# Optimization experiments

Hardware: AMD Instinct MI355X
Metric: run time of the kernel (lower is better)

Reference implementation:

```python
import jax, jax.numpy as jnp
import numpy as np

N_NODES = 100000
N_REL = 4
N_EDGES = 160000  # per relation
IN_F, HID_F, OUT_F = 128, 128, 64


def hetero_layer(x, edges, W, b):
    """Sum over relations of GraphConv (norm='both'): D_in^-1/2 A_r D_out^-1/2 X W_r + b_r."""
    N = x.shape[0]
    out = jnp.zeros((N, W.shape[2]), dtype=x.dtype)
    for r in range(W.shape[0]):  # small fixed relation count
        src = edges[r, 0]
        dst = edges[r, 1]
        ones = jnp.ones(src.shape[0], dtype=x.dtype)
        deg_out = jnp.clip(jax.ops.segment_sum(ones, src, num_segments=N), 1.0)
        deg_in = jnp.clip(jax.ops.segment_sum(ones, dst, num_segments=N), 1.0)
        # scale src features, project (W first since in_feats >= out_feats), gather, scatter-sum
        h = (x * jax.lax.rsqrt(deg_out)[:, None]) @ W[r]
        agg = jax.ops.segment_sum(h[src], dst, num_segments=N)
        out = out + agg * jax.lax.rsqrt(deg_in)[:, None] + b[r]
    return out


def setup_inputs() -> dict:
    key = jax.random.key(0)
    ks = jax.random.split(key, 6)
    x = jax.random.normal(ks[0], (N_NODES, IN_F), dtype=jnp.float32)
    edges = jax.random.randint(ks[1], (N_REL, 2, N_EDGES), 0, N_NODES, dtype=jnp.int32)
    W1 = jax.random.normal(ks[2], (N_REL, IN_F, HID_F), dtype=jnp.float32) * 0.05
    b1 = jnp.zeros((N_REL, HID_F), dtype=jnp.float32)
    W2 = jax.random.normal(ks[3], (N_REL, HID_F, OUT_F), dtype=jnp.float32) * 0.05
    b2 = jnp.zeros((N_REL, OUT_F), dtype=jnp.float32)
    return {"x": x, "edges": edges, "W1": W1, "b1": b1, "W2": W2, "b2": b2}


def reference(x, edges, W1, b1, W2, b2):
    h = jax.nn.relu(hetero_layer(x, edges, W1, b1))
    return hetero_layer(h, edges, W2, b2)
```

## Files before the change

kernel.cpp:

```cpp
#include <hip/hip_runtime.h>
#include <cstddef>
#include <cstdint>

#define NN   100000
#define NR   4
#define NE   160000
#define SCAN_B 1024
#define GEMMB 512

typedef short bf16x8 __attribute__((ext_vector_type(8)));
typedef float f32x4  __attribute__((ext_vector_type(4)));

__device__ __forceinline__ unsigned short f2bf(float f) {
  union { float f; unsigned u; } v; v.f = f;
  unsigned r = v.u + 0x7fffu + ((v.u >> 16) & 1u);
  return (unsigned short)(r >> 16);
}
__device__ __forceinline__ float bf2f(unsigned short h) {
  union { unsigned u; float f; } v; v.u = ((unsigned)h) << 16;
  return v.f;
}

__device__ __forceinline__ void gll16(const unsigned short* g, unsigned short* l) {
  __builtin_amdgcn_global_load_lds(
      (const __attribute__((address_space(1))) void*)g,
      (__attribute__((address_space(3))) void*)l, 16, 0, 0);
}

#define A_ZERO 782
#define A_NBLK (A_ZERO + 6250 + 256 + 128 + 1)
__global__ __launch_bounds__(256) void phaseA_k(const float* __restrict__ x,
                                                const float* __restrict__ W1,
                                                const float* __restrict__ W2,
                                                const float* __restrict__ b1,
                                                const float* __restrict__ b2,
                                                int* __restrict__ cnt,
                                                unsigned short* __restrict__ xb,
                                                unsigned short* __restrict__ Wt1,
                                                unsigned short* __restrict__ Wt2,
                                                float* __restrict__ bs1,
                                                float* __restrict__ bs2) {
  const int bid = blockIdx.x;
  const int t = threadIdx.x;
  if (bid < A_ZERO) {
    const int i = bid * 256 + t;
    if (i < 2 * NR * NN / 4) ((int4*)cnt)[i] = make_int4(0, 0, 0, 0);
  } else if (bid < A_ZERO + 6250) {
    const int i = (bid - A_ZERO) * 256 + t;
    const float4 a = *(const float4*)&x[(size_t)i * 8];
    const float4 b = *(const float4*)&x[(size_t)i * 8 + 4];
    unsigned short o[8];
    o[0] = f2bf(a.x); o[1] = f2bf(a.y); o[2] = f2bf(a.z); o[3] = f2bf(a.w);
    o[4] = f2bf(b.x); o[5] = f2bf(b.y); o[6] = f2bf(b.z); o[7] = f2bf(b.w);
    *(bf16x8*)&xb[(size_t)i * 8] = *(bf16x8*)o;
  } else if (bid < A_ZERO + 6250 + 256) {
    const int i = (bid - A_ZERO - 6250) * 256 + t;
    const int r = i / (128 * 128);
    const int k = (i / 128) % 128;
    const int n = i % 128;
    Wt1[((size_t)r * 128 + n) * 128 + k] = f2bf(W1[i]);
  } else if (bid < A_ZERO + 6250 + 256 + 128) {
    const int i = (bid - A_ZERO - 6250 - 256) * 256 + t;
    const int r = i / (128 * 64);
    const int k = (i / 64) % 128;
    const int n = i % 64;
    Wt2[((size_t)r * 64 + n) * 128 + k] = f2bf(W2[i]);
  } else {
    if (t < 128) bs1[t] = b1[t] + b1[128 + t] + b1[256 + t] + b1[384 + t];
    if (t < 64)  bs2[t] = b2[t] + b2[64 + t] + b2[128 + t] + b2[192 + t];
  }
}

template <int NOUT>
__device__ __forceinline__ void gemm_core(const unsigned short* __restrict__ Xb,
                                          const unsigned short* __restrict__ Wtr,
                                          unsigned short* __restrict__ Hr,
                                          int vb, unsigned short (*Xl)[64 * 128]) {
  const int t = threadIdx.x;
  const int wid = t >> 6;
  const int lane = t & 63;
  const int lg = lane >> 4;
  const int lr = lane & 15;

  constexpr int NF = (NOUT == 128) ? 4 : 2;
  const int rbase = (wid & 1) * 32;
  const int cbase = (wid >> 1) * (NOUT / 2);

  bf16x8 bw[NF][4];
#pragma unroll
  for (int nf = 0; nf < NF; ++nf)
#pragma unroll
    for (int ks = 0; ks < 4; ++ks)
      bw[nf][ks] = *(const bf16x8*)&Wtr[(size_t)(cbase + nf * 16 + lr) * 128 + ks * 32 + lg * 8];

  auto stage = [&](int buf, int tile) {
    const int row0 = tile * 64;
#pragma unroll
    for (int i = 0; i < 4; ++i) {
      const int rl = wid * 16 + i * 4 + (lane >> 4);
      int gr = row0 + rl;
      if (gr >= NN) gr = NN - 1;
      const int q = (lane & 15) ^ (rl & 7);
      gll16(&Xb[(size_t)gr * 128 + q * 8], &Xl[buf][rl * 128 + (lane & 15) * 8]);
    }
  };

  const int ntiles = (NN + 63) / 64;
  int tile = vb;
  stage(0, tile);
  __syncthreads();
  int buf = 0;

  for (; tile < ntiles; tile += 128) {
    const int nxt = tile + 128;
    if (nxt < ntiles) stage(buf ^ 1, nxt);

    f32x4 acc[2][NF];
#pragma unroll
    for (int mf = 0; mf < 2; ++mf)
#pragma unroll
      for (int nf = 0; nf < NF; ++nf) acc[mf][nf] = (f32x4){0.f, 0.f, 0.f, 0.f};

#pragma unroll
    for (int ks = 0; ks < 4; ++ks) {
#pragma unroll
      for (int mf = 0; mf < 2; ++mf) {
        const int r = rbase + mf * 16 + lr;
        const bf16x8 a =
            *(const bf16x8*)&Xl[buf][r * 128 + (((ks * 4 + lg) ^ (lr & 7)) << 3)];
#pragma unroll
        for (int nf = 0; nf < NF; ++nf)
          acc[mf][nf] = __builtin_amdgcn_mfma_f32_16x16x32_bf16(a, bw[nf][ks], acc[mf][nf], 0, 0, 0);
      }
    }

    const int row0 = tile * 64;
#pragma unroll
    for (int mf = 0; mf < 2; ++mf) {
#pragma unroll
      for (int i = 0; i < 4; ++i) {
        const int row = row0 + rbase + mf * 16 + lg * 4 + i;
        if (row < NN) {
#pragma unroll
          for (int nf = 0; nf < NF; ++nf)
            Hr[(size_t)row * NOUT + cbase + nf * 16 + lr] = f2bf(acc[mf][nf][i]);
        }
      }
    }
    __syncthreads();
    buf ^= 1;
  }
}

__device__ __forceinline__ void gemm_dual_core64(const unsigned short* __restrict__ Xb,
                                                 const unsigned short* __restrict__ W0,
                                                 const unsigned short* __restrict__ W1,
                                                 unsigned short* __restrict__ H0,
                                                 unsigned short* __restrict__ H1,
                                                 int vb, unsigned short (*Xl)[64 * 128]) {
  const int t = threadIdx.x;
  const int wid = t >> 6;
  const int lane = t & 63;
  const int lg = lane >> 4;
  const int lr = lane & 15;

  const int rbase = (wid & 1) * 32;
  const int cbase = (wid >> 1) * 32;

  bf16x8 bw[2][2][4];
#pragma unroll
  for (int nf = 0; nf < 2; ++nf)
#pragma unroll
    for (int ks = 0; ks < 4; ++ks) {
      bw[0][nf][ks] = *(const bf16x8*)&W0[(size_t)(cbase + nf * 16 + lr) * 128 + ks * 32 + lg * 8];
      bw[1][nf][ks] = *(const bf16x8*)&W1[(size_t)(cbase + nf * 16 + lr) * 128 + ks * 32 + lg * 8];
    }

  auto stage = [&](int buf, int tile) {
    const int row0 = tile * 64;
#pragma unroll
    for (int i = 0; i < 4; ++i) {
      const int rl = wid * 16 + i * 4 + (lane >> 4);
      int gr = row0 + rl;
      if (gr >= NN) gr = NN - 1;
      const int q = (lane & 15) ^ (rl & 7);
      gll16(&Xb[(size_t)gr * 128 + q * 8], &Xl[buf][rl * 128 + (lane & 15) * 8]);
    }
  };

  const int ntiles = (NN + 63) / 64;
  int tile = vb;
  stage(0, tile);
  __syncthreads();
  int buf = 0;

  for (; tile < ntiles; tile += 128) {
    const int nxt = tile + 128;
    if (nxt < ntiles) stage(buf ^ 1, nxt);

    f32x4 acc[2][2][2];
#pragma unroll
    for (int mf = 0; mf < 2; ++mf)
#pragma unroll
      for (int rel = 0; rel < 2; ++rel)
#pragma unroll
        for (int nf = 0; nf < 2; ++nf) acc[mf][rel][nf] = (f32x4){0.f, 0.f, 0.f, 0.f};

#pragma unroll
    for (int ks = 0; ks < 4; ++ks) {
#pragma unroll
      for (int mf = 0; mf < 2; ++mf) {
        const int r = rbase + mf * 16 + lr;
        const bf16x8 a =
            *(const bf16x8*)&Xl[buf][r * 128 + (((ks * 4 + lg) ^ (lr & 7)) << 3)];
#pragma unroll
        for (int rel = 0; rel < 2; ++rel)
#pragma unroll
          for (int nf = 0; nf < 2; ++nf)
            acc[mf][rel][nf] = __builtin_amdgcn_mfma_f32_16x16x32_bf16(a, bw[rel][nf][ks], acc[mf][rel][nf], 0, 0, 0);
      }
    }

    const int row0 = tile * 64;
#pragma unroll
    for (int mf = 0; mf < 2; ++mf) {
#pragma unroll
      for (int i = 0; i < 4; ++i) {
        const int row = row0 + rbase + mf * 16 + lg * 4 + i;
        if (row < NN) {
#pragma unroll
          for (int nf = 0; nf < 2; ++nf) {
            H0[(size_t)row * 64 + cbase + nf * 16 + lr] = f2bf(acc[mf][0][nf][i]);
            H1[(size_t)row * 64 + cbase + nf * 16 + lr] = f2bf(acc[mf][1][nf][i]);
          }
        }
      }
    }
    __syncthreads();
    buf ^= 1;
  }
}

__global__ __launch_bounds__(256, 2) void phaseB_k(const int* __restrict__ edges,
                                                   const unsigned short* __restrict__ xb,
                                                   const unsigned short* __restrict__ Wt1,
                                                   unsigned short* __restrict__ H,
                                                   int* __restrict__ cnt_out,
                                                   int* __restrict__ cnt_in) {
  __shared__ unsigned short Xl[2][64 * 128];
  const int bid = blockIdx.x;
  if (bid < GEMMB) {
    const int z = bid >> 7;
    gemm_core<128>(xb, Wt1 + (size_t)z * 128 * 128, H + (size_t)z * NN * 128, bid & 127, Xl);
    return;
  }
  const int idx = bid - GEMMB;
  const int r = idx / 625;
  const int e = (idx - r * 625) * 256 + threadIdx.x;
  const int s = edges[(size_t)r * 2 * NE + e];
  const int d = edges[(size_t)r * 2 * NE + NE + e];
  atomicAdd(&cnt_out[(size_t)r * NN + s], 1);
  atomicAdd(&cnt_in[(size_t)r * NN + d], 1);
}

__global__ __launch_bounds__(256, 2) void gemm_dual_k(const unsigned short* __restrict__ Xb,
                                                      const unsigned short* __restrict__ Wt,
                                                      unsigned short* __restrict__ H) {
  __shared__ unsigned short Xl[2][64 * 128];
  const int zp = blockIdx.z;
  gemm_dual_core64(Xb,
                   Wt + (size_t)(2 * zp) * 64 * 128,
                   Wt + (size_t)(2 * zp + 1) * 64 * 128,
                   H + (size_t)(2 * zp) * NN * 64,
                   H + (size_t)(2 * zp + 1) * NN * 64,
                   blockIdx.x, Xl);
}

__global__ __launch_bounds__(256) void scan1_k(const int* __restrict__ cnt_in,
                                               int* __restrict__ excl,
                                               int* __restrict__ bsum) {
  const int b = blockIdx.x, t = threadIdx.x;
  const int base = b * SCAN_B;
  int v[4]; int tl = 0;
#pragma unroll
  for (int i = 0; i < 4; ++i) {
    const int idx = base + t * 4 + i;
    int c = 0;
    if (idx < NN) {
      c = cnt_in[idx] + cnt_in[NN + idx] + cnt_in[2 * NN + idx] + cnt_in[3 * NN + idx];
    }
    v[i] = c;
    tl += c;
  }
  __shared__ int sm[256];
  sm[t] = tl;
  __syncthreads();
  for (int off = 1; off < 256; off <<= 1) {
    const int x = (t >= off) ? sm[t - off] : 0;
    __syncthreads();
    sm[t] += x;
    __syncthreads();
  }
  const int incl = sm[t];
  int run = incl - tl;
#pragma unroll
  for (int i = 0; i < 4; ++i) {
    const int idx = base + t * 4 + i;
    if (idx < NN) excl[idx] = run;
    run += v[i];
  }
  if (t == 255) bsum[b] = incl;
}

__global__ __launch_bounds__(128) void scan2_k(int* __restrict__ bsum, int nb) {
  const int t = threadIdx.x;
  __shared__ int sm[128];
  const int v = (t < nb) ? bsum[t] : 0;
  sm[t] = v;
  __syncthreads();
  for (int off = 1; off < 128; off <<= 1) {
    const int x = (t >= off) ? sm[t - off] : 0;
    __syncthreads();
    sm[t] += x;
    __syncthreads();
  }
  if (t < nb) bsum[t] = sm[t] - v;
}

__global__ __launch_bounds__(256) void scan3rs_k(const int* __restrict__ cnt,
                                                 float* __restrict__ rs,
                                                 const int* __restrict__ bsum,
                                                 int* __restrict__ row_ptr,
                                                 int* __restrict__ cursor) {
  const int bid = blockIdx.x, t = threadIdx.x;
  if (bid < 3125) {
    const int i = bid * 256 + t;
    rs[i] = rsqrtf(fmaxf((float)cnt[i], 1.0f));
  } else {
    const int i = (bid - 3125) * 256 + t;
    if (i < NN) {
      const int v = cursor[i] + bsum[i / SCAN_B];
      row_ptr[i] = v;
      cursor[i] = v;
    }
    if (i == 0) row_ptr[NN] = NR * NE;
  }
}

__global__ __launch_bounds__(256) void fill_k(const int* __restrict__ edges,
                                              const float* __restrict__ rs_out,
                                              const float* __restrict__ rs_in,
                                              int* __restrict__ cursor,
                                              int2* __restrict__ csr) {
  const int r = blockIdx.y;
  const int e = blockIdx.x * 256 + threadIdx.x;
  if (e >= NE) return;
  const int s = edges[(size_t)r * 2 * NE + e];
  const int d = edges[(size_t)r * 2 * NE + NE + e];
  const int pos = atomicAdd(&cursor[d], 1);
  const float w = rs_in[(size_t)r * NN + d] * rs_out[(size_t)r * NN + s];
  csr[pos] = make_int2(r * NN + s, __float_as_int(w));
}

__global__ __launch_bounds__(256) void gather1_k(const unsigned short* __restrict__ H,
                                                 const int* __restrict__ row_ptr,
                                                 const int2* __restrict__ csr,
                                                 const float* __restrict__ bs1,
                                                 unsigned short* __restrict__ h1b) {
  const int node = blockIdx.x * 4 + (threadIdx.x >> 6);
  const int lane = threadIdx.x & 63;
  if (node >= NN) return;
  const int g  = lane >> 4;
  const int fl = lane & 15;

  float acc[8];
#pragma unroll
  for (int j = 0; j < 8; ++j) acc[j] = 0.f;

  const int beg = row_ptr[node];
  const int end = row_ptr[node + 1];
  for (int e = beg + g; e < end; e += 4) {
    const int2 p = csr[e];
    const float w = __int_as_float(p.y);
    const bf16x8 h = *(const bf16x8*)&H[(size_t)p.x * 128 + fl * 8];
#pragma unroll
    for (int j = 0; j < 8; ++j)
      acc[j] = fmaf(bf2f((unsigned short)h[j]), w, acc[j]);
  }
#pragma unroll
  for (int j = 0; j < 8; ++j) {
    acc[j] += __shfl_xor(acc[j], 16);
    acc[j] += __shfl_xor(acc[j], 32);
  }
  if (g == 0) {
    const float4 c0 = *(const float4*)&bs1[fl * 8];
    const float4 c1 = *(const float4*)&bs1[fl * 8 + 4];
    unsigned short o[8];
    o[0] = f2bf(fmaxf(acc[0] + c0.x, 0.f));
    o[1] = f2bf(fmaxf(acc[1] + c0.y, 0.f));
    o[2] = f2bf(fmaxf(acc[2] + c0.z, 0.f));
    o[3] = f2bf(fmaxf(acc[3] + c0.w, 0.f));
    o[4] = f2bf(fmaxf(acc[4] + c1.x, 0.f));
    o[5] = f2bf(fmaxf(acc[5] + c1.y, 0.f));
    o[6] = f2bf(fmaxf(acc[6] + c1.z, 0.f));
    o[7] = f2bf(fmaxf(acc[7] + c1.w, 0.f));
    *(bf16x8*)&h1b[(size_t)node * 128 + fl * 8] = *(bf16x8*)o;
  }
}

__global__ __launch_bounds__(256) void gather2_k(const unsigned short* __restrict__ H,
                                                 const int* __restrict__ row_ptr,
                                                 const int2* __restrict__ csr,
                                                 const float* __restrict__ bs2,
                                                 float* __restrict__ out) {
  const int node = blockIdx.x * 4 + (threadIdx.x >> 6);
  const int lane = threadIdx.x & 63;
  if (node >= NN) return;
  const int g  = lane >> 3;
  const int fl = lane & 7;

  float acc[8];
#pragma unroll
  for (int j = 0; j < 8; ++j) acc[j] = 0.f;

  const int beg = row_ptr[node];
  const int end = row_ptr[node + 1];
  for (int e = beg + g; e < end; e += 8) {
    const int2 p = csr[e];
    const float w = __int_as_float(p.y);
    const bf16x8 h = *(const bf16x8*)&H[(size_t)p.x * 64 + fl * 8];
#pragma unroll
    for (int j = 0; j < 8; ++j)
      acc[j] = fmaf(bf2f((unsigned short)h[j]), w, acc[j]);
  }
#pragma unroll
  for (int j = 0; j < 8; ++j) {
    acc[j] += __shfl_xor(acc[j], 8);
    acc[j] += __shfl_xor(acc[j], 16);
    acc[j] += __shfl_xor(acc[j], 32);
  }
  if (g == 0) {
    const float4 c0 = *(const float4*)&bs2[fl * 8];
    const float4 c1 = *(const float4*)&bs2[fl * 8 + 4];
    float4 o0, o1;
    o0.x = acc[0] + c0.x; o0.y = acc[1] + c0.y; o0.z = acc[2] + c0.z; o0.w = acc[3] + c0.w;
    o1.x = acc[4] + c1.x; o1.y = acc[5] + c1.y; o1.z = acc[6] + c1.z; o1.w = acc[7] + c1.w;
    *(float4*)&out[(size_t)node * 64 + fl * 8]     = o0;
    *(float4*)&out[(size_t)node * 64 + fl * 8 + 4] = o1;
  }
}

extern "C" void kernel_launch(void* const* d_in, const int* in_sizes, int n_in,
                              void* d_out, int out_size, void* d_ws, size_t ws_size,
                              hipStream_t stream) {
  const float* x     = (const float*)d_in[0];
  const int*   edges = (const int*)d_in[1];
  const float* W1    = (const float*)d_in[2];
  const float* b1    = (const float*)d_in[3];
  const float* W2    = (const float*)d_in[4];
  const float* b2    = (const float*)d_in[5];
  float* out = (float*)d_out;

  unsigned short* xb   = (unsigned short*)d_ws;
  unsigned short* h1b  = xb;
  unsigned short* Hbuf = xb + (size_t)NN * 128;
  unsigned short* Wt1  = Hbuf + (size_t)NR * NN * 128;
  unsigned short* Wt2  = Wt1 + (size_t)NR * 128 * 128;
  float* rs_out = (float*)(Wt2 + (size_t)NR * 64 * 128);
  float* rs_in  = rs_out + (size_t)NR * NN;
  int* cnt_out  = (int*)(rs_in + (size_t)NR * NN);
  int* cnt_in   = cnt_out + (size_t)NR * NN;
  int* row_ptr  = cnt_in + (size_t)NR * NN;
  int* cursor   = row_ptr + (NN + 1);
  int* bsum     = cursor + NN;
  float* bs1    = (float*)(bsum + 128);
  float* bs2    = bs1 + 128;
  int2* csr     = (int2*)(bs2 + 64);

  const int nb = (NN + SCAN_B - 1) / SCAN_B;

  phaseA_k<<<A_NBLK, 256, 0, stream>>>(x, W1, W2, b1, b2, cnt_out, xb, Wt1, Wt2, bs1, bs2);
  phaseB_k<<<GEMMB + 2500, 256, 0, stream>>>(edges, xb, Wt1, Hbuf, cnt_out, cnt_in);
  scan1_k<<<nb, 256, 0, stream>>>(cnt_in, cursor , bsum);
  scan2_k<<<1, 128, 0, stream>>>(bsum, nb);
  scan3rs_k<<<3125 + (NN + 255) / 256, 256, 0, stream>>>(cnt_out, rs_out, bsum, row_ptr, cursor);
  fill_k<<<dim3((NE + 255) / 256, NR), 256, 0, stream>>>(edges, rs_out, rs_in, cursor, csr);
  gather1_k<<<(NN + 3) / 4, 256, 0, stream>>>(Hbuf, row_ptr, csr, bs1, h1b);
  gemm_dual_k<<<dim3(128, 1, 2), 256, 0, stream>>>(h1b, Wt2, Hbuf);
  gather2_k<<<(NN + 3) / 4, 256, 0, stream>>>(Hbuf, row_ptr, csr, bs2, out);
}
```

Baseline: 217.1 us.

## Shard degree counters across copies and use per-relation CSR fill cursors

Degree counting now spreads its atomics over four replicated counter arrays, chosen by block index, to cut same-address contention. The scan and rs kernels reduce across the shards, and the fill step uses a separate cursor per relation and destination so fewer atomics collide on one node. The CSR buffer now reuses the counter workspace, and zeroing covers four times as much memory. This adds reduction reads and a larger memset in exchange for less atomic serialization.

After: 221.1 us. About the same (+1.9%).

```diff
diff --git a/kernel.cpp b/kernel.cpp
--- a/kernel.cpp
+++ b/kernel.cpp
@@ -7,6 +7,7 @@
 #define NE   160000
 #define SCAN_B 1024
 #define GEMMB 512
+#define SH   4
 
 typedef short bf16x8 __attribute__((ext_vector_type(8)));
 typedef float f32x4  __attribute__((ext_vector_type(4)));
@@ -27,7 +28,7 @@
       (__attribute__((address_space(3))) void*)l, 16, 0, 0);
 }
 
-#define A_ZERO 782
+#define A_ZERO 3125
 #define A_NBLK (A_ZERO + 6250 + 256 + 128 + 1)
 __global__ __launch_bounds__(256) void phaseA_k(const float* __restrict__ x,
                                                 const float* __restrict__ W1,
@@ -44,7 +45,7 @@
   const int t = threadIdx.x;
   if (bid < A_ZERO) {
     const int i = bid * 256 + t;
-    if (i < 2 * NR * NN / 4) ((int4*)cnt)[i] = make_int4(0, 0, 0, 0);
+    ((int4*)cnt)[i] = make_int4(0, 0, 0, 0);
   } else if (bid < A_ZERO + 6250) {
     const int i = (bid - A_ZERO) * 256 + t;
     const float4 a = *(const float4*)&x[(size_t)i * 8];
@@ -245,8 +246,8 @@
                                                    const unsigned short* __restrict__ xb,
                                                    const unsigned short* __restrict__ Wt1,
                                                    unsigned short* __restrict__ H,
-                                                   int* __restrict__ cnt_out,
-                                                   int* __restrict__ cnt_in) {
+                                                   int* __restrict__ cntO,
+                                                   int* __restrict__ cntI) {
   __shared__ unsigned short Xl[2][64 * 128];
   const int bid = blockIdx.x;
   if (bid < GEMMB) {
@@ -256,11 +257,12 @@
   }
   const int idx = bid - GEMMB;
   const int r = idx / 625;
+  const int sh = idx & (SH - 1);
   const int e = (idx - r * 625) * 256 + threadIdx.x;
   const int s = edges[(size_t)r * 2 * NE + e];
   const int d = edges[(size_t)r * 2 * NE + NE + e];
-  atomicAdd(&cnt_out[(size_t)r * NN + s], 1);
-  atomicAdd(&cnt_in[(size_t)r * NN + d], 1);
+  atomicAdd(&cntO[((size_t)sh * NR + r) * NN + s], 1);
+  atomicAdd(&cntI[((size_t)sh * NR + r) * NN + d], 1);
 }
 
 __global__ __launch_bounds__(256, 2) void gemm_dual_k(const unsigned short* __restrict__ Xb,
@@ -276,7 +278,7 @@
                    blockIdx.x, Xl);
 }
 
-__global__ __launch_bounds__(256) void scan1_k(const int* __restrict__ cnt_in,
+__global__ __launch_bounds__(256) void scan1_k(const int* __restrict__ cntI,
                                                int* __restrict__ excl,
                                                int* __restrict__ bsum) {
   const int b = blockIdx.x, t = threadIdx.x;
@@ -287,7 +289,11 @@
     const int idx = base + t * 4 + i;
     int c = 0;
     if (idx < NN) {
-      c = cnt_in[idx] + cnt_in[NN + idx] + cnt_in[2 * NN + idx] + cnt_in[3 * NN + idx];
+#pragma unroll
+      for (int sh = 0; sh < SH; ++sh) {
+        const size_t o = (size_t)sh * NR * NN + idx;
+        c += cntI[o] + cntI[o + NN] + cntI[o + 2 * NN] + cntI[o + 3 * NN];
+      }
     }
     v[i] = c;
     tl += c;
@@ -327,21 +333,46 @@
   if (t < nb) bsum[t] = sm[t] - v;
 }
 
-__global__ __launch_bounds__(256) void scan3rs_k(const int* __restrict__ cnt,
-                                                 float* __restrict__ rs,
+__global__ __launch_bounds__(256) void scan3rs_k(const int* __restrict__ cntO,
+                                                 const int* __restrict__ cntI,
+                                                 float* __restrict__ rs_out,
+                                                 float* __restrict__ rs_in,
+                                                 const int* __restrict__ excl,
                                                  const int* __restrict__ bsum,
                                                  int* __restrict__ row_ptr,
-                                                 int* __restrict__ cursor) {
+                                                 int* __restrict__ cursorR) {
   const int bid = blockIdx.x, t = threadIdx.x;
   if (bid < 3125) {
     const int i = bid * 256 + t;
-    rs[i] = rsqrtf(fmaxf((float)cnt[i], 1.0f));
+    if (i < NR * NN) {
+      int c = 0;
+#pragma unroll
+      for (int sh = 0; sh < SH; ++sh) c += cntO[(size_t)sh * NR * NN + i];
+      rs_out[i] = rsqrtf(fmaxf((float)c, 1.0f));
+    } else {
+      const int j = i - NR * NN;
+      int c = 0;
+#pragma unroll
+      for (int sh = 0; sh < SH; ++sh) c += cntI[(size_t)sh * NR * NN + j];
+      rs_in[j] = rsqrtf(fmaxf((float)c, 1.0f));
+    }
   } else {
     const int i = (bid - 3125) * 256 + t;
     if (i < NN) {
-      const int v = cursor[i] + bsum[i / SCAN_B];
-      row_ptr[i] = v;
-      cursor[i] = v;
+      const int base = excl[i] + bsum[i / SCAN_B];
+      int c[NR];
+#pragma unroll
+      for (int r = 0; r < NR; ++r) {
+        int s = 0;
+#pragma unroll
+        for (int sh = 0; sh < SH; ++sh) s += cntI[((size_t)sh * NR + r) * NN + i];
+        c[r] = s;
+      }
+      row_ptr[i] = base;
+      cursorR[i]            = base;
+      cursorR[NN + i]       = base + c[0];
+      cursorR[2 * NN + i]   = base + c[0] + c[1];
+      cursorR[3 * NN + i]   = base + c[0] + c[1] + c[2];
     }
     if (i == 0) row_ptr[NN] = NR * NE;
   }
@@ -350,14 +381,14 @@
 __global__ __launch_bounds__(256) void fill_k(const int* __restrict__ edges,
                                               const float* __restrict__ rs_out,
                                               const float* __restrict__ rs_in,
-                                              int* __restrict__ cursor,
+                                              int* __restrict__ cursorR,
                                               int2* __restrict__ csr) {
   const int r = blockIdx.y;
   const int e = blockIdx.x * 256 + threadIdx.x;
   if (e >= NE) return;
   const int s = edges[(size_t)r * 2 * NE + e];
   const int d = edges[(size_t)r * 2 * NE + NE + e];
-  const int pos = atomicAdd(&cursor[d], 1);
+  const int pos = atomicAdd(&cursorR[(size_t)r * NN + d], 1);
   const float w = rs_in[(size_t)r * NN + d] * rs_out[(size_t)r * NN + s];
   csr[pos] = make_int2(r * NN + s, __float_as_int(w));
 }
@@ -468,23 +499,25 @@
   unsigned short* Wt2  = Wt1 + (size_t)NR * 128 * 128;
   float* rs_out = (float*)(Wt2 + (size_t)NR * 64 * 128);
   float* rs_in  = rs_out + (size_t)NR * NN;
-  int* cnt_out  = (int*)(rs_in + (size_t)NR * NN);
-  int* cnt_in   = cnt_out + (size_t)NR * NN;
-  int* row_ptr  = cnt_in + (size_t)NR * NN;
-  int* cursor   = row_ptr + (NN + 1);
-  int* bsum     = cursor + NN;
+  int* cntO     = (int*)(rs_in + (size_t)NR * NN);
+  int* cntI     = cntO + (size_t)SH * NR * NN;
+  int* row_ptr  = cntI + (size_t)SH * NR * NN;
+  int* excl     = row_ptr + (NN + 1);
+  int* cursorR  = excl + NN;
+  int* bsum     = cursorR + (size_t)NR * NN;
   float* bs1    = (float*)(bsum + 128);
   float* bs2    = bs1 + 128;
-  int2* csr     = (int2*)(bs2 + 64);
+  int2* csr     = (int2*)cntO;
 
   const int nb = (NN + SCAN_B - 1) / SCAN_B;
 
-  phaseA_k<<<A_NBLK, 256, 0, stream>>>(x, W1, W2, b1, b2, cnt_out, xb, Wt1, Wt2, bs1, bs2);
-  phaseB_k<<<GEMMB + 2500, 256, 0, stream>>>(edges, xb, Wt1, Hbuf, cnt_out, cnt_in);
-  scan1_k<<<nb, 256, 0, stream>>>(cnt_in, cursor , bsum);
+  phaseA_k<<<A_NBLK, 256, 0, stream>>>(x, W1, W2, b1, b2, cntO, xb, Wt1, Wt2, bs1, bs2);
+  phaseB_k<<<GEMMB + 2500, 256, 0, stream>>>(edges, xb, Wt1, Hbuf, cntO, cntI);
+  scan1_k<<<nb, 256, 0, stream>>>(cntI, excl, bsum);
   scan2_k<<<1, 128, 0, stream>>>(bsum, nb);
-  scan3rs_k<<<3125 + (NN + 255) / 256, 256, 0, stream>>>(cnt_out, rs_out, bsum, row_ptr, cursor);
-  fill_k<<<dim3((NE + 255) / 256, NR), 256, 0, stream>>>(edges, rs_out, rs_in, cursor, csr);
+  scan3rs_k<<<3125 + (NN + 255) / 256, 256, 0, stream>>>(cntO, cntI, rs_out, rs_in,
+                                                         excl, bsum, row_ptr, cursorR);
+  fill_k<<<dim3((NE + 255) / 256, NR), 256, 0, stream>>>(edges, rs_out, rs_in, cursorR, csr);
   gather1_k<<<(NN + 3) / 4, 256, 0, stream>>>(Hbuf, row_ptr, csr, bs1, h1b);
   gemm_dual_k<<<dim3(128, 1, 2), 256, 0, stream>>>(h1b, Wt2, Hbuf);
   gather2_k<<<(NN + 3) / 4, 256, 0, stream>>>(Hbuf, row_ptr, csr, bs2, out);
```

## Merge scan kernels, use per-relation cursors, and preload CSR edges via shuffles

Applied to the files above, without the earlier changes.

Folds the block-sum scan into the row-pointer kernel so each block redundantly scans the small block-sum array, and moves the rs_in computation into the first scan, dropping one launch. Fill now uses separate per-relation cursors, which spreads atomics across four counters per destination and cuts contention. The gather kernels load up to 64 CSR entries per node in one coalesced wavefront load and broadcast them with shuffles, taking edge-index loads off the dependent chain. The cost is extra cursor memory, a redundant small scan in every block, and a branch for nodes with more than 64 edges.

Result: no change. 214.4 us (-1.2%).

```diff
diff --git a/kernel.cpp b/kernel.cpp
--- a/kernel.cpp
+++ b/kernel.cpp
@@ -276,21 +276,35 @@
                    blockIdx.x, Xl);
 }
 
-__global__ __launch_bounds__(256) void scan1_k(const int* __restrict__ cnt_in,
+__global__ __launch_bounds__(256) void scanA_k(const int* __restrict__ cnt_in,
                                                int* __restrict__ excl,
-                                               int* __restrict__ bsum) {
+                                               int* __restrict__ bsum,
+                                               float* __restrict__ rs_in,
+                                               int* __restrict__ cursorR) {
   const int b = blockIdx.x, t = threadIdx.x;
   const int base = b * SCAN_B;
   int v[4]; int tl = 0;
 #pragma unroll
   for (int i = 0; i < 4; ++i) {
     const int idx = base + t * 4 + i;
-    int c = 0;
+    int tot = 0;
     if (idx < NN) {
-      c = cnt_in[idx] + cnt_in[NN + idx] + cnt_in[2 * NN + idx] + cnt_in[3 * NN + idx];
-    }
-    v[i] = c;
-    tl += c;
+      const int c0 = cnt_in[idx];
+      const int c1 = cnt_in[NN + idx];
+      const int c2 = cnt_in[2 * NN + idx];
+      const int c3 = cnt_in[3 * NN + idx];
+      tot = c0 + c1 + c2 + c3;
+      rs_in[idx]          = rsqrtf(fmaxf((float)c0, 1.0f));
+      rs_in[NN + idx]     = rsqrtf(fmaxf((float)c1, 1.0f));
+      rs_in[2 * NN + idx] = rsqrtf(fmaxf((float)c2, 1.0f));
+      rs_in[3 * NN + idx] = rsqrtf(fmaxf((float)c3, 1.0f));
+      cursorR[idx]          = 0;
+      cursorR[NN + idx]     = c0;
+      cursorR[2 * NN + idx] = c0 + c1;
+      cursorR[3 * NN + idx] = c0 + c1 + c2;
+    }
+    v[i] = tot;
+    tl += tot;
   }
   __shared__ int sm[256];
   sm[t] = tl;
@@ -312,52 +326,59 @@
   if (t == 255) bsum[b] = incl;
 }
 
-__global__ __launch_bounds__(128) void scan2_k(int* __restrict__ bsum, int nb) {
-  const int t = threadIdx.x;
-  __shared__ int sm[128];
-  const int v = (t < nb) ? bsum[t] : 0;
-  sm[t] = v;
+__global__ __launch_bounds__(256) void scanB_k(const int* __restrict__ cnt_out,
+                                               float* __restrict__ rs_out,
+                                               const int* __restrict__ excl,
+                                               const int* __restrict__ bsum,
+                                               int* __restrict__ row_ptr,
+                                               int* __restrict__ cursorR, int nb) {
+  const int bid = blockIdx.x, t = threadIdx.x;
+  if (bid < 1563) {
+    const int i = bid * 256 + t;
+    if (i < NR * NN) rs_out[i] = rsqrtf(fmaxf((float)cnt_out[i], 1.0f));
+    return;
+  }
+  __shared__ int sb[128];
+  __shared__ int se[128];
+  int myv = 0;
+  if (t < 128) {
+    myv = (t < nb) ? bsum[t] : 0;
+    sb[t] = myv;
+  }
   __syncthreads();
   for (int off = 1; off < 128; off <<= 1) {
-    const int x = (t >= off) ? sm[t - off] : 0;
+    int x = 0;
+    if (t < 128 && t >= off) x = sb[t - off];
     __syncthreads();
-    sm[t] += x;
+    if (t < 128) sb[t] += x;
     __syncthreads();
   }
-  if (t < nb) bsum[t] = sm[t] - v;
-}
-
-__global__ __launch_bounds__(256) void scan3rs_k(const int* __restrict__ cnt,
-                                                 float* __restrict__ rs,
-                                                 const int* __restrict__ bsum,
-                                                 int* __restrict__ row_ptr,
-                                                 int* __restrict__ cursor) {
-  const int bid = blockIdx.x, t = threadIdx.x;
-  if (bid < 3125) {
-    const int i = bid * 256 + t;
-    rs[i] = rsqrtf(fmaxf((float)cnt[i], 1.0f));
-  } else {
-    const int i = (bid - 3125) * 256 + t;
-    if (i < NN) {
-      const int v = cursor[i] + bsum[i / SCAN_B];
-      row_ptr[i] = v;
-      cursor[i] = v;
-    }
-    if (i == 0) row_ptr[NN] = NR * NE;
-  }
+  if (t < 128) se[t] = sb[t] - myv;
+  __syncthreads();
+
+  const int i = (bid - 1563) * 256 + t;
+  if (i < NN) {
+    const int rb = excl[i] + se[i / SCAN_B];
+    row_ptr[i] = rb;
+    cursorR[i]          += rb;
+    cursorR[NN + i]     += rb;
+    cursorR[2 * NN + i] += rb;
+    cursorR[3 * NN + i] += rb;
+  }
+  if (i == 0) row_ptr[NN] = NR * NE;
 }
 
 __global__ __launch_bounds__(256) void fill_k(const int* __restrict__ edges,
                                               const float* __restrict__ rs_out,
                                               const float* __restrict__ rs_in,
-                                              int* __restrict__ cursor,
+                                              int* __restrict__ cursorR,
                                               int2* __restrict__ csr) {
   const int r = blockIdx.y;
   const int e = blockIdx.x * 256 + threadIdx.x;
   if (e >= NE) return;
   const int s = edges[(size_t)r * 2 * NE + e];
   const int d = edges[(size_t)r * 2 * NE + NE + e];
-  const int pos = atomicAdd(&cursor[d], 1);
+  const int pos = atomicAdd(&cursorR[(size_t)r * NN + d], 1);
   const float w = rs_in[(size_t)r * NN + d] * rs_out[(size_t)r * NN + s];
   csr[pos] = make_int2(r * NN + s, __float_as_int(w));
 }
@@ -373,19 +394,39 @@
   const int g  = lane >> 4;
   const int fl = lane & 15;
 
-  float acc[8];
-#pragma unroll
-  for (int j = 0; j < 8; ++j) acc[j] = 0.f;
-
   const int beg = row_ptr[node];
   const int end = row_ptr[node + 1];
-  for (int e = beg + g; e < end; e += 4) {
-    const int2 p = csr[e];
-    const float w = __int_as_float(p.y);
-    const bf16x8 h = *(const bf16x8*)&H[(size_t)p.x * 128 + fl * 8];
-#pragma unroll
-    for (int j = 0; j < 8; ++j)
-      acc[j] = fmaf(bf2f((unsigned short)h[j]), w, acc[j]);
+  const int deg = end - beg;
+
+  int2 p = make_int2(0, 0);
+  if (lane < deg) p = csr[beg + lane];
+
+  float acc[8];
+#pragma unroll
+  for (int j = 0; j < 8; ++j) acc[j] = 0.f;
+
+  if (deg <= 64) {
+    const int kmax = (deg + 3) >> 2;
+    for (int k = 0; k < kmax; ++k) {
+      const int e = g + k * 4;
+      const int row = __shfl(p.x, e);
+      const float w = __int_as_float(__shfl(p.y, e));
+      if (e < deg) {
+        const bf16x8 h = *(const bf16x8*)&H[(size_t)row * 128 + fl * 8];
+#pragma unroll
+        for (int j = 0; j < 8; ++j)
+          acc[j] = fmaf(bf2f((unsigned short)h[j]), w, acc[j]);
+      }
+    }
+  } else {
+    for (int e = beg + g; e < end; e += 4) {
+      const int2 q = csr[e];
+      const float w = __int_as_float(q.y);
+      const bf16x8 h = *(const bf16x8*)&H[(size_t)q.x * 128 + fl * 8];
+#pragma unroll
+      for (int j = 0; j < 8; ++j)
+        acc[j] = fmaf(bf2f((unsigned short)h[j]), w, acc[j]);
+    }
   }
 #pragma unroll
   for (int j = 0; j < 8; ++j) {
@@ -419,19 +460,39 @@
   const int g  = lane >> 3;
   const int fl = lane & 7;
 
-  float acc[8];
-#pragma unroll
-  for (int j = 0; j < 8; ++j) acc[j] = 0.f;
-
   const int beg = row_ptr[node];
   const int end = row_ptr[node + 1];
-  for (int e = beg + g; e < end; e += 8) {
-    const int2 p = csr[e];
-    const float w = __int_as_float(p.y);
-    const bf16x8 h = *(const bf16x8*)&H[(size_t)p.x * 64 + fl * 8];
-#pragma unroll
-    for (int j = 0; j < 8; ++j)
-      acc[j] = fmaf(bf2f((unsigned short)h[j]), w, acc[j]);
+  const int deg = end - beg;
+
+  int2 p = make_int2(0, 0);
+  if (lane < deg) p = csr[beg + lane];
+
+  float acc[8];
+#pragma unroll
+  for (int j = 0; j < 8; ++j) acc[j] = 0.f;
+
+  if (deg <= 64) {
+    const int kmax = (deg + 7) >> 3;
+    for (int k = 0; k < kmax; ++k) {
+      const int e = g + k * 8;
+      const int row = __shfl(p.x, e);
+      const float w = __int_as_float(__shfl(p.y, e));
+      if (e < deg) {
+        const bf16x8 h = *(const bf16x8*)&H[(size_t)row * 64 + fl * 8];
+#pragma unroll
+        for (int j = 0; j < 8; ++j)
+          acc[j] = fmaf(bf2f((unsigned short)h[j]), w, acc[j]);
+      }
+    }
+  } else {
+    for (int e = beg + g; e < end; e += 8) {
+      const int2 q = csr[e];
+      const float w = __int_as_float(q.y);
+      const bf16x8 h = *(const bf16x8*)&H[(size_t)q.x * 64 + fl * 8];
+#pragma unroll
+      for (int j = 0; j < 8; ++j)
+        acc[j] = fmaf(bf2f((unsigned short)h[j]), w, acc[j]);
+    }
   }
 #pragma unroll
   for (int j = 0; j < 8; ++j) {
@@ -471,8 +532,9 @@
   int* cnt_out  = (int*)(rs_in + (size_t)NR * NN);
   int* cnt_in   = cnt_out + (size_t)NR * NN;
   int* row_ptr  = cnt_in + (size_t)NR * NN;
-  int* cursor   = row_ptr + (NN + 1);
-  int* bsum     = cursor + NN;
+  int* excl     = row_ptr + (NN + 1);
+  int* cursorR  = excl + NN;
+  int* bsum     = cursorR + (size_t)NR * NN;
   float* bs1    = (float*)(bsum + 128);
   float* bs2    = bs1 + 128;
   int2* csr     = (int2*)(bs2 + 64);
@@ -481,10 +543,10 @@
 
   phaseA_k<<<A_NBLK, 256, 0, stream>>>(x, W1, W2, b1, b2, cnt_out, xb, Wt1, Wt2, bs1, bs2);
   phaseB_k<<<GEMMB + 2500, 256, 0, stream>>>(edges, xb, Wt1, Hbuf, cnt_out, cnt_in);
-  scan1_k<<<nb, 256, 0, stream>>>(cnt_in, cursor , bsum);
-  scan2_k<<<1, 128, 0, stream>>>(bsum, nb);
-  scan3rs_k<<<3125 + (NN + 255) / 256, 256, 0, stream>>>(cnt_out, rs_out, bsum, row_ptr, cursor);
-  fill_k<<<dim3((NE + 255) / 256, NR), 256, 0, stream>>>(edges, rs_out, rs_in, cursor, csr);
+  scanA_k<<<nb, 256, 0, stream>>>(cnt_in, excl, bsum, rs_in, cursorR);
+  scanB_k<<<1563 + (NN + 255) / 256, 256, 0, stream>>>(cnt_out, rs_out, excl, bsum,
+                                                       row_ptr, cursorR, nb);
+  fill_k<<<dim3((NE + 255) / 256, NR), 256, 0, stream>>>(edges, rs_out, rs_in, cursorR, csr);
   gather1_k<<<(NN + 3) / 4, 256, 0, stream>>>(Hbuf, row_ptr, csr, bs1, h1b);
   gemm_dual_k<<<dim3(128, 1, 2), 256, 0, stream>>>(h1b, Wt2, Hbuf);
   gather2_k<<<(NN + 3) / 4, 256, 0, stream>>>(Hbuf, row_ptr, csr, bs2, out);
```
